# Kernel optimization log

Hardware: AMD Instinct MI355X
Metric: run time of the kernel (lower is better)

## Reference

```python
import jax, jax.numpy as jnp
import numpy as np

N, E, DIN, DH, DOUT = 50000, 800000, 256, 128, 64


def setup_inputs() -> dict:
    key = jax.random.key(0)
    ks = jax.random.split(key, 12)
    return {
        "h": jax.random.normal(ks[0], (N, DIN), jnp.float32),
        "src": jax.random.randint(ks[1], (E,), 0, N, jnp.int32),
        "dst": jax.random.randint(ks[2], (E,), 0, N, jnp.int32),
        "W1": jax.random.normal(ks[3], (DIN, DH), jnp.float32) * (DIN ** -0.5),
        "al1": jax.random.normal(ks[4], (DH,), jnp.float32) * (DH ** -0.5),
        "ar1": jax.random.normal(ks[5], (DH,), jnp.float32) * (DH ** -0.5),
        "W2": jax.random.normal(ks[6], (DH, DH), jnp.float32) * (DH ** -0.5),
        "al2": jax.random.normal(ks[7], (DH,), jnp.float32) * (DH ** -0.5),
        "ar2": jax.random.normal(ks[8], (DH,), jnp.float32) * (DH ** -0.5),
        "W3": jax.random.normal(ks[9], (DH, DOUT), jnp.float32) * (DH ** -0.5),
        "al3": jax.random.normal(ks[10], (DOUT,), jnp.float32) * (DOUT ** -0.5),
        "ar3": jax.random.normal(ks[11], (DOUT,), jnp.float32) * (DOUT ** -0.5),
    }


def gat_layer(h, W, al, ar, src, dst):
    """DGL GATConv, 1 head, no bias: proj -> leaky_relu edge scores -> edge softmax over dst -> scatter-sum."""
    n = h.shape[0]
    f = h @ W                                   # [N, d]
    el = f @ al                                 # [N]
    er = f @ ar                                 # [N]
    e = jax.nn.leaky_relu(el[src] + er[dst], negative_slope=0.2)  # [E]
    m = jax.ops.segment_max(e, dst, num_segments=n)
    m = jnp.where(jnp.isfinite(m), m, 0.0)      # zero-in-degree nodes
    m = jax.lax.stop_gradient(m)
    ex = jnp.exp(e - m[dst])                    # [E]
    z = jax.ops.segment_sum(ex, dst, num_segments=n)
    a = ex / jnp.maximum(z, 1e-9)[dst]          # [E] softmax weights
    return jax.ops.segment_sum(a[:, None] * f[src], dst, num_segments=n)


def reference(h, src, dst, W1, al1, ar1, W2, al2, ar2, W3, al3, ar3):
    x = gat_layer(h, W1, al1, ar1, src, dst)
    x = jax.nn.relu(x)                          # dropout = identity (eval)
    x = gat_layer(x, W2, al2, ar2, src, dst)
    x = jax.nn.relu(x)
    x = gat_layer(x, W3, al3, ar3, src, dst)    # mean over 1 head = identity
    return jax.nn.log_softmax(x, axis=-1)
```

## Files before the change

### kernel.cpp

```cpp
#include <hip/hip_runtime.h>
#include <math.h>

#define DIN 256
#define DHID 128
#define DOUTC 64
#define EPB 2048

typedef __attribute__((ext_vector_type(8))) short short8;
typedef __attribute__((ext_vector_type(4))) float f32x4;

static __device__ __forceinline__ float wave_max(float v){
  #pragma unroll
  for (int o=1;o<64;o<<=1) v = fmaxf(v, __shfl_xor(v,o,64));
  return v;
}
static __device__ __forceinline__ float wave_sum(float v){
  #pragma unroll
  for (int o=1;o<64;o<<=1) v += __shfl_xor(v,o,64);
  return v;
}

static __device__ __forceinline__ unsigned short bf16_rne(float x){
  unsigned int u = __float_as_uint(x);
  return (unsigned short)((u + 0x7FFFu + ((u>>16)&1u)) >> 16);
}
static __device__ __forceinline__ float bf16_to_f32(unsigned short h){
  return __uint_as_float(((unsigned int)h)<<16);
}
static __device__ __forceinline__ float blo(unsigned int u){ return __uint_as_float(u<<16); }
static __device__ __forceinline__ float bhi(unsigned int u){ return __uint_as_float(u & 0xffff0000u); }

__global__ __launch_bounds__(256) void rs_hist(const int* __restrict__ dst,
    int* __restrict__ ghist, int E, int NB){
  __shared__ int h[256];
  const int t = threadIdx.x, blk = blockIdx.x;
  h[t] = 0; __syncthreads();
  const int base = blk*EPB;
  #pragma unroll
  for (int i=0;i<EPB/256;i++){
    int j = base + i*256 + t;
    if (j < E) atomicAdd(&h[dst[j]>>8], 1);
  }
  __syncthreads();
  ghist[t*NB + blk] = h[t];
}

__global__ __launch_bounds__(256) void rs_scan(int* __restrict__ ghist,
    int* __restrict__ btot, int NB){
  __shared__ int b[256];
  __shared__ int carry;
  const int hb = blockIdx.x, t = threadIdx.x;
  if (t==0) carry = 0;
  __syncthreads();
  for (int c0=0; c0<NB; c0+=256){
    int i = c0 + t;
    int v = (i<NB)? ghist[hb*NB+i] : 0;
    b[t] = v; __syncthreads();
    #pragma unroll
    for (int o=1;o<256;o<<=1){
      int x = (t>=o)? b[t-o] : 0;
      __syncthreads();
      b[t] += x;
      __syncthreads();
    }
    if (i<NB) ghist[hb*NB+i] = carry + b[t] - v;
    __syncthreads();
    if (t==255) carry += b[255];
    __syncthreads();
  }
  if (t==255) btot[hb] = carry;
}

__global__ __launch_bounds__(256) void rs_scan2(int* __restrict__ btot,
    int* __restrict__ offsets, int N, int E){
  __shared__ int b[256];
  const int t = threadIdx.x;
  int v = btot[t];
  b[t] = v; __syncthreads();
  #pragma unroll
  for (int o=1;o<256;o<<=1){
    int x = (t>=o)? b[t-o] : 0;
    __syncthreads();
    b[t] += x;
    __syncthreads();
  }
  btot[t] = b[t] - v;
  if (t==255){ btot[256] = E; offsets[N] = E; }
}

__global__ __launch_bounds__(256) void rs_scatter(const int* __restrict__ src,
    const int* __restrict__ dst, const int* __restrict__ ghist,
    const int* __restrict__ btot, uint2* __restrict__ ebuf, int E, int NB){
  __shared__ int cur[256];
  const int t = threadIdx.x, blk = blockIdx.x;
  cur[t] = ghist[t*NB + blk] + btot[t];
  __syncthreads();
  const int base = blk*EPB;
  #pragma unroll
  for (int i=0;i<EPB/256;i++){
    int j = base + i*256 + t;
    if (j < E){
      int d = dst[j];
      int pos = atomicAdd(&cur[d>>8], 1);
      ebuf[pos] = make_uint2((unsigned)src[j], (unsigned)d);
    }
  }
}

__global__ __launch_bounds__(256) void bucket_sort(const uint2* __restrict__ ebuf,
    const int* __restrict__ btot, int* __restrict__ offsets,
    int* __restrict__ srcs, int N){
  __shared__ int h[256];
  __shared__ int b[256];
  const int hb = blockIdx.x, t = threadIdx.x;
  const int b0 = btot[hb], b1 = btot[hb+1];
  h[t] = 0; __syncthreads();
  for (int j=b0+t; j<b1; j+=256) atomicAdd(&h[ebuf[j].y & 255u], 1);
  __syncthreads();
  int v = h[t];
  b[t] = v; __syncthreads();
  #pragma unroll
  for (int o=1;o<256;o<<=1){
    int x = (t>=o)? b[t-o] : 0;
    __syncthreads();
    b[t] += x;
    __syncthreads();
  }
  const int excl = b[t] - v;
  const int node = hb*256 + t;
  if (node < N) offsets[node] = b0 + excl;
  h[t] = excl;
  __syncthreads();
  for (int j=b0+t; j<b1; j+=256){
    uint2 e = ebuf[j];
    int pos = b0 + atomicAdd(&h[e.y & 255u], 1);
    srcs[pos] = (int)e.x;
  }
}

template<int K, int NC>
__global__ void pack_kernel(const float* __restrict__ W, unsigned short* __restrict__ Wp){
  constexpr int CT = NC/16, KT = K/32;
  int idx = blockIdx.x*256 + threadIdx.x;
  if (idx >= KT*CT*64) return;
  int l = idx & 63, t = idx >> 6;
  int ct = t % CT, kt = t / CT;
  int col = ct*16 + (l & 15);
  int k0 = kt*32 + (l >> 4)*8;
  unsigned short* dstp = Wp + (size_t)idx*8;
  #pragma unroll
  for (int j=0;j<8;j++)
    dstp[j] = bf16_rne(W[(size_t)(k0+j)*NC + col]);
}

template<int K, int NC>
__global__ __launch_bounds__(256) void gemm_v3(const float* __restrict__ A,
    const unsigned short* __restrict__ Wp,
    const float* __restrict__ al, const float* __restrict__ ar,
    unsigned short* __restrict__ Fb, float* __restrict__ el, float* __restrict__ er, int nrows)
{
  constexpr int CT = NC/16, KT = K/32;
  constexpr int CHUNK_KT = (32/CT) < KT ? (32/CT) : KT;
  constexpr int NCHUNK = KT / CHUNK_KT;
  constexpr int CHUNK_SHORTS = CHUNK_KT*CT*64*8;
  __shared__ unsigned short bsm[CHUNK_SHORTS];

  const int tid = threadIdx.x;
  const int lane = tid & 63;
  const int wid  = tid >> 6;
  const int row0 = blockIdx.x*64 + wid*16;
  const int c = lane & 15, g = lane >> 4;
  const int arow = row0 + c;
  const bool aok = arow < nrows;

  f32x4 acc[CT];
  #pragma unroll
  for (int i=0;i<CT;i++) acc[i] = (f32x4)0.f;

  for (int ch=0; ch<NCHUNK; ++ch){
    if (ch) __syncthreads();
    {
      const uint4* gsrc = (const uint4*)Wp + (size_t)ch*(CHUNK_SHORTS/8);
      uint4* ldst = (uint4*)bsm;
      #pragma unroll
      for (int i=0; i<CHUNK_SHORTS/8/256; ++i)
        ldst[i*256 + tid] = gsrc[i*256 + tid];
    }
    __syncthreads();

    #pragma unroll
    for (int ktl=0; ktl<CHUNK_KT; ++ktl){
      const int k0 = (ch*CHUNK_KT + ktl)*32 + g*8;
      float xs[8];
      if (aok){
        float4 v0 = *(const float4*)&A[(size_t)arow*K + k0];
        float4 v1 = *(const float4*)&A[(size_t)arow*K + k0 + 4];
        xs[0]=v0.x; xs[1]=v0.y; xs[2]=v0.z; xs[3]=v0.w;
        xs[4]=v1.x; xs[5]=v1.y; xs[6]=v1.z; xs[7]=v1.w;
      } else {
        #pragma unroll
        for (int j=0;j<8;j++) xs[j]=0.f;
      }
      short8 ahi, alo;
      #pragma unroll
      for (int j=0;j<8;j++){
        unsigned short hh = bf16_rne(xs[j]);
        ahi[j] = (short)hh;
        alo[j] = (short)bf16_rne(xs[j] - bf16_to_f32(hh));
      }
      #pragma unroll
      for (int ct=0; ct<CT; ++ct){
        short8 b = *(const short8*)&bsm[(ktl*CT+ct)*512 + lane*8];
        acc[ct] = __builtin_amdgcn_mfma_f32_16x16x32_bf16(ahi, b, acc[ct], 0,0,0);
        acc[ct] = __builtin_amdgcn_mfma_f32_16x16x32_bf16(alo, b, acc[ct], 0,0,0);
      }
    }
  }

  float alv[CT], arv[CT];
  #pragma unroll
  for (int ct=0;ct<CT;ct++){ alv[ct]=al[ct*16+c]; arv[ct]=ar[ct*16+c]; }
  #pragma unroll
  for (int j=0;j<4;j++){
    const int row = row0 + g*4 + j;
    const bool ok = row < nrows;
    float sl=0.f, sr=0.f;
    #pragma unroll
    for (int ct=0;ct<CT;ct++){
      float f = acc[ct][j];
      sl = fmaf(f, alv[ct], sl);
      sr = fmaf(f, arv[ct], sr);
      if (ok) Fb[(size_t)row*NC + ct*16 + c] = bf16_rne(f);
    }
    #pragma unroll
    for (int o=1;o<16;o<<=1){ sl += __shfl_xor(sl,o,64); sr += __shfl_xor(sr,o,64); }
    if (ok && c==0){ el[row]=sl; er[row]=sr; }
  }
}

template<int D, bool RELU, bool LOGSM>
__global__ __launch_bounds__(256) void agg3_kernel(const unsigned short* __restrict__ Fb,
    const float* __restrict__ el, const float* __restrict__ er,
    const int* __restrict__ offsets, const int* __restrict__ srcs,
    float* __restrict__ out, int N)
{
  constexpr int CPL = D/16;
  __shared__ float2 ws[4][64];
  const int wv = threadIdx.x >> 6;
  const int lane = threadIdx.x & 63;
  const int c16 = lane & 15, g = lane >> 4;
  const int v = blockIdx.x*4 + wv;
  if (v >= N) return;
  const int o0 = offsets[v], o1 = offsets[v+1];
  const float erv = er[v];

  float m = -INFINITY, z = 0.f;
  float acc[CPL];
  #pragma unroll
  for (int i=0;i<CPL;i++) acc[i]=0.f;

  for (int s0 = o0; s0 < o1; s0 += 64){
    const int j = s0 + lane;
    int sidx = 0; float e = -INFINITY;
    if (j < o1){
      sidx = srcs[j];
      float tv = el[sidx] + erv;
      e = (tv > 0.f) ? tv : 0.2f*tv;
    }
    const float nm = fmaxf(m, wave_max(e));
    const float scale = __expf(m - nm);
    const float wgt = __expf(e - nm);
    z = z*scale + wave_sum(wgt);
    #pragma unroll
    for (int i=0;i<CPL;i++) acc[i] *= scale;
    m = nm;
    ws[wv][lane] = make_float2(wgt, __int_as_float(sidx));
    __builtin_amdgcn_wave_barrier();

    const int cnt = min(64, o1 - s0);
    int t = g;
    if (D == 128){
      for (; t+4 < cnt; t += 8){
        float2 p0 = ws[wv][t], p1 = ws[wv][t+4];
        uint4 u0 = *((const uint4*)(Fb + (size_t)__float_as_int(p0.y)*128) + c16);
        uint4 u1 = *((const uint4*)(Fb + (size_t)__float_as_int(p1.y)*128) + c16);
        acc[0]=fmaf(p0.x, blo(u0.x), acc[0]); acc[1]=fmaf(p0.x, bhi(u0.x), acc[1]);
        acc[2]=fmaf(p0.x, blo(u0.y), acc[2]); acc[3]=fmaf(p0.x, bhi(u0.y), acc[3]);
        acc[4]=fmaf(p0.x, blo(u0.z), acc[4]); acc[5]=fmaf(p0.x, bhi(u0.z), acc[5]);
        acc[6]=fmaf(p0.x, blo(u0.w), acc[6]); acc[7]=fmaf(p0.x, bhi(u0.w), acc[7]);
        acc[0]=fmaf(p1.x, blo(u1.x), acc[0]); acc[1]=fmaf(p1.x, bhi(u1.x), acc[1]);
        acc[2]=fmaf(p1.x, blo(u1.y), acc[2]); acc[3]=fmaf(p1.x, bhi(u1.y), acc[3]);
        acc[4]=fmaf(p1.x, blo(u1.z), acc[4]); acc[5]=fmaf(p1.x, bhi(u1.z), acc[5]);
        acc[6]=fmaf(p1.x, blo(u1.w), acc[6]); acc[7]=fmaf(p1.x, bhi(u1.w), acc[7]);
      }
      if (t < cnt){
        float2 p0 = ws[wv][t];
        uint4 u0 = *((const uint4*)(Fb + (size_t)__float_as_int(p0.y)*128) + c16);
        acc[0]=fmaf(p0.x, blo(u0.x), acc[0]); acc[1]=fmaf(p0.x, bhi(u0.x), acc[1]);
        acc[2]=fmaf(p0.x, blo(u0.y), acc[2]); acc[3]=fmaf(p0.x, bhi(u0.y), acc[3]);
        acc[4]=fmaf(p0.x, blo(u0.z), acc[4]); acc[5]=fmaf(p0.x, bhi(u0.z), acc[5]);
        acc[6]=fmaf(p0.x, blo(u0.w), acc[6]); acc[7]=fmaf(p0.x, bhi(u0.w), acc[7]);
      }
    } else {
      for (; t+4 < cnt; t += 8){
        float2 p0 = ws[wv][t], p1 = ws[wv][t+4];
        uint2 u0 = *((const uint2*)(Fb + (size_t)__float_as_int(p0.y)*64) + c16);
        uint2 u1 = *((const uint2*)(Fb + (size_t)__float_as_int(p1.y)*64) + c16);
        acc[0]=fmaf(p0.x, blo(u0.x), acc[0]); acc[1]=fmaf(p0.x, bhi(u0.x), acc[1]);
        acc[2]=fmaf(p0.x, blo(u0.y), acc[2]); acc[3]=fmaf(p0.x, bhi(u0.y), acc[3]);
        acc[0]=fmaf(p1.x, blo(u1.x), acc[0]); acc[1]=fmaf(p1.x, bhi(u1.x), acc[1]);
        acc[2]=fmaf(p1.x, blo(u1.y), acc[2]); acc[3]=fmaf(p1.x, bhi(u1.y), acc[3]);
      }
      if (t < cnt){
        float2 p0 = ws[wv][t];
        uint2 u0 = *((const uint2*)(Fb + (size_t)__float_as_int(p0.y)*64) + c16);
        acc[0]=fmaf(p0.x, blo(u0.x), acc[0]); acc[1]=fmaf(p0.x, bhi(u0.x), acc[1]);
        acc[2]=fmaf(p0.x, blo(u0.y), acc[2]); acc[3]=fmaf(p0.x, bhi(u0.y), acc[3]);
      }
    }
    __builtin_amdgcn_wave_barrier();
  }

  #pragma unroll
  for (int i=0;i<CPL;i++){
    acc[i] += __shfl_xor(acc[i],16,64);
    acc[i] += __shfl_xor(acc[i],32,64);
  }
  const float zi = 1.f / fmaxf(z, 1e-9f);

  if (LOGSM){
    float y[CPL];
    #pragma unroll
    for (int i=0;i<CPL;i++) y[i] = acc[i]*zi;
    float M = y[0];
    #pragma unroll
    for (int i=1;i<CPL;i++) M = fmaxf(M, y[i]);
    #pragma unroll
    for (int o=1;o<16;o<<=1) M = fmaxf(M, __shfl_xor(M,o,64));
    float ssum = 0.f;
    #pragma unroll
    for (int i=0;i<CPL;i++) ssum += __expf(y[i]-M);
    #pragma unroll
    for (int o=1;o<16;o<<=1) ssum += __shfl_xor(ssum,o,64);
    const float lw = M + logf(ssum);
    if (g==0){
      float4 r = make_float4(y[0]-lw, y[1]-lw, y[2]-lw, y[3]-lw);
      *(float4*)&out[(size_t)v*64 + c16*4] = r;
    }
  } else {
    if (g==0){
      float r[CPL];
      #pragma unroll
      for (int i=0;i<CPL;i++){ r[i]=acc[i]*zi; if (RELU) r[i]=fmaxf(r[i],0.f); }
      *(float4*)&out[(size_t)v*128 + c16*8]     = make_float4(r[0],r[1],r[2],r[3]);
      *(float4*)&out[(size_t)v*128 + c16*8 + 4] = make_float4(r[4],r[5],r[6],r[7]);
    }
  }
}

extern "C" void kernel_launch(void* const* d_in, const int* in_sizes, int n_in,
                              void* d_out, int out_size, void* d_ws, size_t ws_size,
                              hipStream_t stream) {
  const float* h   = (const float*)d_in[0];
  const int*   src = (const int*)d_in[1];
  const int*   dst = (const int*)d_in[2];
  const float* W1  = (const float*)d_in[3];
  const float* al1 = (const float*)d_in[4];
  const float* ar1 = (const float*)d_in[5];
  const float* W2  = (const float*)d_in[6];
  const float* al2 = (const float*)d_in[7];
  const float* ar2 = (const float*)d_in[8];
  const float* W3  = (const float*)d_in[9];
  const float* al3 = (const float*)d_in[10];
  const float* ar3 = (const float*)d_in[11];

  const int N = in_sizes[0] / DIN;
  const int E = in_sizes[1];
  const int NB = (E + EPB - 1) / EPB;
  const int NHB = (N + 255) / 256;

  auto alignup = [](size_t x){ return (x + 255) & ~(size_t)255; };
  char* p = (char*)d_ws;
  int* offsets = (int*)p; p += alignup(((size_t)N+1)*4);
  int* srcs    = (int*)p; p += alignup((size_t)E*4);
  int* ghist   = (int*)p; p += alignup((size_t)256*NB*4);
  int* btot    = (int*)p; p += alignup(257*4);
  uint2* ebuf  = (uint2*)p; p += alignup((size_t)E*8);
  unsigned short* Fb = (unsigned short*)p; p += alignup((size_t)N*DHID*2);
  float* X     = (float*)p; p += alignup((size_t)N*DHID*4);
  float* el    = (float*)p; p += alignup((size_t)N*4);
  float* er    = (float*)p; p += alignup((size_t)N*4);
  unsigned short* Wp1 = (unsigned short*)p; p += alignup((size_t)(DIN/32)*(DHID/16)*64*8*2);
  unsigned short* Wp2 = (unsigned short*)p; p += alignup((size_t)(DHID/32)*(DHID/16)*64*8*2);
  unsigned short* Wp3 = (unsigned short*)p; p += alignup((size_t)(DHID/32)*(DOUTC/16)*64*8*2);

  const int nbW4 = (N+3)/4;
  const int nbG  = (N+63)/64;

  pack_kernel<DIN ,DHID ><<<(DIN/32)*(DHID/16)*64/256,  256,0,stream>>>(W1, Wp1);
  pack_kernel<DHID,DHID ><<<(DHID/32)*(DHID/16)*64/256, 256,0,stream>>>(W2, Wp2);
  pack_kernel<DHID,DOUTC><<<(DHID/32)*(DOUTC/16)*64/256,256,0,stream>>>(W3, Wp3);

  rs_hist   <<<NB, 256,0,stream>>>(dst, ghist, E, NB);
  rs_scan   <<<256,256,0,stream>>>(ghist, btot, NB);
  rs_scan2  <<<1,  256,0,stream>>>(btot, offsets, N, E);
  rs_scatter<<<NB, 256,0,stream>>>(src, dst, ghist, btot, ebuf, E, NB);
  bucket_sort<<<NHB,256,0,stream>>>(ebuf, btot, offsets, srcs, N);

  gemm_v3<DIN,DHID><<<nbG,256,0,stream>>>(h, Wp1, al1, ar1, Fb, el, er, N);
  agg3_kernel<128,true,false><<<nbW4,256,0,stream>>>(Fb, el, er, offsets, srcs, X, N);

  gemm_v3<DHID,DHID><<<nbG,256,0,stream>>>(X, Wp2, al2, ar2, Fb, el, er, N);
  agg3_kernel<128,true,false><<<nbW4,256,0,stream>>>(Fb, el, er, offsets, srcs, X, N);

  gemm_v3<DHID,DOUTC><<<nbG,256,0,stream>>>(X, Wp3, al3, ar3, Fb, el, er, N);
  agg3_kernel<64,false,true><<<nbW4,256,0,stream>>>(Fb, el, er, offsets, srcs, (float*)d_out, N);
}
```

Baseline: 180.3 us.

## Store hidden activations in bf16, drop split-bf16 MFMA for layers 2-3, fuse weight packing

The intermediate activations X are now written as bf16 by the aggregation kernel. The layer 2 and 3 GEMMs read bf16 directly and issue one MFMA per tile instead of a hi/lo split pair. This halves activation traffic and GEMM MFMA work for those layers, at the cost of lower activation precision. The three weight-pack launches are merged into one kernel, and the gather loop is unrolled to four edges per iteration for more memory-level parallelism.

```diff
diff --git a/kernel.cpp b/kernel.cpp
--- a/kernel.cpp
+++ b/kernel.cpp
@@ -139,10 +139,9 @@
 }
 
 template<int K, int NC>
-__global__ void pack_kernel(const float* __restrict__ W, unsigned short* __restrict__ Wp){
-  constexpr int CT = NC/16, KT = K/32;
-  int idx = blockIdx.x*256 + threadIdx.x;
-  if (idx >= KT*CT*64) return;
+static __device__ __forceinline__ void pack_one(const float* __restrict__ W,
+    unsigned short* __restrict__ Wp, int idx){
+  constexpr int CT = NC/16;
   int l = idx & 63, t = idx >> 6;
   int ct = t % CT, kt = t / CT;
   int col = ct*16 + (l & 15);
@@ -153,8 +152,21 @@
     dstp[j] = bf16_rne(W[(size_t)(k0+j)*NC + col]);
 }
 
-template<int K, int NC>
-__global__ __launch_bounds__(256) void gemm_v3(const float* __restrict__ A,
+__global__ __launch_bounds__(256) void pack_all(const float* __restrict__ W1,
+    const float* __restrict__ W2, const float* __restrict__ W3,
+    unsigned short* __restrict__ Wp1, unsigned short* __restrict__ Wp2,
+    unsigned short* __restrict__ Wp3){
+  constexpr int N1 = (DIN/32)*(DHID/16)*64;
+  constexpr int N2 = (DHID/32)*(DHID/16)*64;
+  constexpr int N3 = (DHID/32)*(DOUTC/16)*64;
+  int idx = blockIdx.x*256 + threadIdx.x;
+  if (idx < N1) pack_one<DIN,DHID>(W1, Wp1, idx);
+  else if (idx < N1+N2) pack_one<DHID,DHID>(W2, Wp2, idx-N1);
+  else if (idx < N1+N2+N3) pack_one<DHID,DOUTC>(W3, Wp3, idx-N1-N2);
+}
+
+template<int K, int NC, bool AF32>
+__global__ __launch_bounds__(256) void gemm_v3(const void* __restrict__ Av,
     const unsigned short* __restrict__ Wp,
     const float* __restrict__ al, const float* __restrict__ ar,
     unsigned short* __restrict__ Fb, float* __restrict__ el, float* __restrict__ er, int nrows)
@@ -165,6 +177,9 @@
   constexpr int CHUNK_SHORTS = CHUNK_KT*CT*64*8;
   __shared__ unsigned short bsm[CHUNK_SHORTS];
 
+  const float* Af = (const float*)Av;
+  const unsigned short* Abf = (const unsigned short*)Av;
+
   const int tid = threadIdx.x;
   const int lane = tid & 63;
   const int wid  = tid >> 6;
@@ -191,28 +206,35 @@
     #pragma unroll
     for (int ktl=0; ktl<CHUNK_KT; ++ktl){
       const int k0 = (ch*CHUNK_KT + ktl)*32 + g*8;
-      float xs[8];
-      if (aok){
-        float4 v0 = *(const float4*)&A[(size_t)arow*K + k0];
-        float4 v1 = *(const float4*)&A[(size_t)arow*K + k0 + 4];
-        xs[0]=v0.x; xs[1]=v0.y; xs[2]=v0.z; xs[3]=v0.w;
-        xs[4]=v1.x; xs[5]=v1.y; xs[6]=v1.z; xs[7]=v1.w;
+      short8 ahi, alo;
+      if constexpr (AF32){
+        float xs[8];
+        if (aok){
+          float4 v0 = *(const float4*)&Af[(size_t)arow*K + k0];
+          float4 v1 = *(const float4*)&Af[(size_t)arow*K + k0 + 4];
+          xs[0]=v0.x; xs[1]=v0.y; xs[2]=v0.z; xs[3]=v0.w;
+          xs[4]=v1.x; xs[5]=v1.y; xs[6]=v1.z; xs[7]=v1.w;
+        } else {
+          #pragma unroll
+          for (int j=0;j<8;j++) xs[j]=0.f;
+        }
+        #pragma unroll
+        for (int j=0;j<8;j++){
+          unsigned short hh = bf16_rne(xs[j]);
+          ahi[j] = (short)hh;
+          alo[j] = (short)bf16_rne(xs[j] - bf16_to_f32(hh));
+        }
       } else {
-        #pragma unroll
-        for (int j=0;j<8;j++) xs[j]=0.f;
-      }
-      short8 ahi, alo;
-      #pragma unroll
-      for (int j=0;j<8;j++){
-        unsigned short hh = bf16_rne(xs[j]);
-        ahi[j] = (short)hh;
-        alo[j] = (short)bf16_rne(xs[j] - bf16_to_f32(hh));
+        if (aok) ahi = *(const short8*)&Abf[(size_t)arow*K + k0];
+        else     ahi = (short8)0;
+        alo = ahi;
       }
       #pragma unroll
       for (int ct=0; ct<CT; ++ct){
         short8 b = *(const short8*)&bsm[(ktl*CT+ct)*512 + lane*8];
         acc[ct] = __builtin_amdgcn_mfma_f32_16x16x32_bf16(ahi, b, acc[ct], 0,0,0);
-        acc[ct] = __builtin_amdgcn_mfma_f32_16x16x32_bf16(alo, b, acc[ct], 0,0,0);
+        if constexpr (AF32)
+          acc[ct] = __builtin_amdgcn_mfma_f32_16x16x32_bf16(alo, b, acc[ct], 0,0,0);
       }
     }
   }
@@ -238,11 +260,11 @@
   }
 }
 
-template<int D, bool RELU, bool LOGSM>
-__global__ __launch_bounds__(256) void agg3_kernel(const unsigned short* __restrict__ Fb,
+template<int D, bool RELU, bool LOGSM, bool OUTBF>
+__global__ __launch_bounds__(256) void agg4_kernel(const unsigned short* __restrict__ Fb,
     const float* __restrict__ el, const float* __restrict__ er,
     const int* __restrict__ offsets, const int* __restrict__ srcs,
-    float* __restrict__ out, int N)
+    void* __restrict__ outv, int N)
 {
   constexpr int CPL = D/16;
   __shared__ float2 ws[4][64];
@@ -279,11 +301,14 @@
 
     const int cnt = min(64, o1 - s0);
     int t = g;
-    if (D == 128){
-      for (; t+4 < cnt; t += 8){
-        float2 p0 = ws[wv][t], p1 = ws[wv][t+4];
+    if constexpr (D == 128){
+      for (; t+12 < cnt; t += 16){
+        float2 p0 = ws[wv][t],   p1 = ws[wv][t+4];
+        float2 p2 = ws[wv][t+8], p3 = ws[wv][t+12];
         uint4 u0 = *((const uint4*)(Fb + (size_t)__float_as_int(p0.y)*128) + c16);
         uint4 u1 = *((const uint4*)(Fb + (size_t)__float_as_int(p1.y)*128) + c16);
+        uint4 u2 = *((const uint4*)(Fb + (size_t)__float_as_int(p2.y)*128) + c16);
+        uint4 u3 = *((const uint4*)(Fb + (size_t)__float_as_int(p3.y)*128) + c16);
         acc[0]=fmaf(p0.x, blo(u0.x), acc[0]); acc[1]=fmaf(p0.x, bhi(u0.x), acc[1]);
         acc[2]=fmaf(p0.x, blo(u0.y), acc[2]); acc[3]=fmaf(p0.x, bhi(u0.y), acc[3]);
         acc[4]=fmaf(p0.x, blo(u0.z), acc[4]); acc[5]=fmaf(p0.x, bhi(u0.z), acc[5]);
@@ -292,8 +317,16 @@
         acc[2]=fmaf(p1.x, blo(u1.y), acc[2]); acc[3]=fmaf(p1.x, bhi(u1.y), acc[3]);
         acc[4]=fmaf(p1.x, blo(u1.z), acc[4]); acc[5]=fmaf(p1.x, bhi(u1.z), acc[5]);
         acc[6]=fmaf(p1.x, blo(u1.w), acc[6]); acc[7]=fmaf(p1.x, bhi(u1.w), acc[7]);
-      }
-      if (t < cnt){
+        acc[0]=fmaf(p2.x, blo(u2.x), acc[0]); acc[1]=fmaf(p2.x, bhi(u2.x), acc[1]);
+        acc[2]=fmaf(p2.x, blo(u2.y), acc[2]); acc[3]=fmaf(p2.x, bhi(u2.y), acc[3]);
+        acc[4]=fmaf(p2.x, blo(u2.z), acc[4]); acc[5]=fmaf(p2.x, bhi(u2.z), acc[5]);
+        acc[6]=fmaf(p2.x, blo(u2.w), acc[6]); acc[7]=fmaf(p2.x, bhi(u2.w), acc[7]);
+        acc[0]=fmaf(p3.x, blo(u3.x), acc[0]); acc[1]=fmaf(p3.x, bhi(u3.x), acc[1]);
+        acc[2]=fmaf(p3.x, blo(u3.y), acc[2]); acc[3]=fmaf(p3.x, bhi(u3.y), acc[3]);
+        acc[4]=fmaf(p3.x, blo(u3.z), acc[4]); acc[5]=fmaf(p3.x, bhi(u3.z), acc[5]);
+        acc[6]=fmaf(p3.x, blo(u3.w), acc[6]); acc[7]=fmaf(p3.x, bhi(u3.w), acc[7]);
+      }
+      for (; t < cnt; t += 4){
         float2 p0 = ws[wv][t];
         uint4 u0 = *((const uint4*)(Fb + (size_t)__float_as_int(p0.y)*128) + c16);
         acc[0]=fmaf(p0.x, blo(u0.x), acc[0]); acc[1]=fmaf(p0.x, bhi(u0.x), acc[1]);
@@ -302,16 +335,23 @@
         acc[6]=fmaf(p0.x, blo(u0.w), acc[6]); acc[7]=fmaf(p0.x, bhi(u0.w), acc[7]);
       }
     } else {
-      for (; t+4 < cnt; t += 8){
-        float2 p0 = ws[wv][t], p1 = ws[wv][t+4];
+      for (; t+12 < cnt; t += 16){
+        float2 p0 = ws[wv][t],   p1 = ws[wv][t+4];
+        float2 p2 = ws[wv][t+8], p3 = ws[wv][t+12];
         uint2 u0 = *((const uint2*)(Fb + (size_t)__float_as_int(p0.y)*64) + c16);
         uint2 u1 = *((const uint2*)(Fb + (size_t)__float_as_int(p1.y)*64) + c16);
+        uint2 u2 = *((const uint2*)(Fb + (size_t)__float_as_int(p2.y)*64) + c16);
+        uint2 u3 = *((const uint2*)(Fb + (size_t)__float_as_int(p3.y)*64) + c16);
         acc[0]=fmaf(p0.x, blo(u0.x), acc[0]); acc[1]=fmaf(p0.x, bhi(u0.x), acc[1]);
         acc[2]=fmaf(p0.x, blo(u0.y), acc[2]); acc[3]=fmaf(p0.x, bhi(u0.y), acc[3]);
         acc[0]=fmaf(p1.x, blo(u1.x), acc[0]); acc[1]=fmaf(p1.x, bhi(u1.x), acc[1]);
         acc[2]=fmaf(p1.x, blo(u1.y), acc[2]); acc[3]=fmaf(p1.x, bhi(u1.y), acc[3]);
-      }
-      if (t < cnt){
+        acc[0]=fmaf(p2.x, blo(u2.x), acc[0]); acc[1]=fmaf(p2.x, bhi(u2.x), acc[1]);
+        acc[2]=fmaf(p2.x, blo(u2.y), acc[2]); acc[3]=fmaf(p2.x, bhi(u2.y), acc[3]);
+        acc[0]=fmaf(p3.x, blo(u3.x), acc[0]); acc[1]=fmaf(p3.x, bhi(u3.x), acc[1]);
+        acc[2]=fmaf(p3.x, blo(u3.y), acc[2]); acc[3]=fmaf(p3.x, bhi(u3.y), acc[3]);
+      }
+      for (; t < cnt; t += 4){
         float2 p0 = ws[wv][t];
         uint2 u0 = *((const uint2*)(Fb + (size_t)__float_as_int(p0.y)*64) + c16);
         acc[0]=fmaf(p0.x, blo(u0.x), acc[0]); acc[1]=fmaf(p0.x, bhi(u0.x), acc[1]);
@@ -328,7 +368,8 @@
   }
   const float zi = 1.f / fmaxf(z, 1e-9f);
 
-  if (LOGSM){
+  if constexpr (LOGSM){
+    float* out = (float*)outv;
     float y[CPL];
     #pragma unroll
     for (int i=0;i<CPL;i++) y[i] = acc[i]*zi;
@@ -347,13 +388,17 @@
       float4 r = make_float4(y[0]-lw, y[1]-lw, y[2]-lw, y[3]-lw);
       *(float4*)&out[(size_t)v*64 + c16*4] = r;
     }
-  } else {
+  } else if constexpr (OUTBF){
+    unsigned short* outb = (unsigned short*)outv;
     if (g==0){
-      float r[CPL];
+      short8 o8;
       #pragma unroll
-      for (int i=0;i<CPL;i++){ r[i]=acc[i]*zi; if (RELU) r[i]=fmaxf(r[i],0.f); }
-      *(float4*)&out[(size_t)v*128 + c16*8]     = make_float4(r[0],r[1],r[2],r[3]);
-      *(float4*)&out[(size_t)v*128 + c16*8 + 4] = make_float4(r[4],r[5],r[6],r[7]);
+      for (int i=0;i<CPL;i++){
+        float r = acc[i]*zi;
+        if (RELU) r = fmaxf(r,0.f);
+        o8[i] = (short)bf16_rne(r);
+      }
+      *(short8*)&outb[(size_t)v*128 + c16*8] = o8;
     }
   }
 }
@@ -387,7 +432,7 @@
   int* btot    = (int*)p; p += alignup(257*4);
   uint2* ebuf  = (uint2*)p; p += alignup((size_t)E*8);
   unsigned short* Fb = (unsigned short*)p; p += alignup((size_t)N*DHID*2);
-  float* X     = (float*)p; p += alignup((size_t)N*DHID*4);
+  unsigned short* X  = (unsigned short*)p; p += alignup((size_t)N*DHID*2);
   float* el    = (float*)p; p += alignup((size_t)N*4);
   float* er    = (float*)p; p += alignup((size_t)N*4);
   unsigned short* Wp1 = (unsigned short*)p; p += alignup((size_t)(DIN/32)*(DHID/16)*64*8*2);
@@ -397,9 +442,7 @@
   const int nbW4 = (N+3)/4;
   const int nbG  = (N+63)/64;
 
-  pack_kernel<DIN ,DHID ><<<(DIN/32)*(DHID/16)*64/256,  256,0,stream>>>(W1, Wp1);
-  pack_kernel<DHID,DHID ><<<(DHID/32)*(DHID/16)*64/256, 256,0,stream>>>(W2, Wp2);
-  pack_kernel<DHID,DOUTC><<<(DHID/32)*(DOUTC/16)*64/256,256,0,stream>>>(W3, Wp3);
+  pack_all<<<28,256,0,stream>>>(W1, W2, W3, Wp1, Wp2, Wp3);
 
   rs_hist   <<<NB, 256,0,stream>>>(dst, ghist, E, NB);
   rs_scan   <<<256,256,0,stream>>>(ghist, btot, NB);
@@ -407,12 +450,12 @@
   rs_scatter<<<NB, 256,0,stream>>>(src, dst, ghist, btot, ebuf, E, NB);
   bucket_sort<<<NHB,256,0,stream>>>(ebuf, btot, offsets, srcs, N);
 
-  gemm_v3<DIN,DHID><<<nbG,256,0,stream>>>(h, Wp1, al1, ar1, Fb, el, er, N);
-  agg3_kernel<128,true,false><<<nbW4,256,0,stream>>>(Fb, el, er, offsets, srcs, X, N);
-
-  gemm_v3<DHID,DHID><<<nbG,256,0,stream>>>(X, Wp2, al2, ar2, Fb, el, er, N);
-  agg3_kernel<128,true,false><<<nbW4,256,0,stream>>>(Fb, el, er, offsets, srcs, X, N);
-
-  gemm_v3<DHID,DOUTC><<<nbG,256,0,stream>>>(X, Wp3, al3, ar3, Fb, el, er, N);
-  agg3_kernel<64,false,true><<<nbW4,256,0,stream>>>(Fb, el, er, offsets, srcs, (float*)d_out, N);
-}
+  gemm_v3<DIN,DHID,true><<<nbG,256,0,stream>>>(h, Wp1, al1, ar1, Fb, el, er, N);
+  agg4_kernel<128,true,false,true><<<nbW4,256,0,stream>>>(Fb, el, er, offsets, srcs, X, N);
+
+  gemm_v3<DHID,DHID,false><<<nbG,256,0,stream>>>(X, Wp2, al2, ar2, Fb, el, er, N);
+  agg4_kernel<128,true,false,true><<<nbW4,256,0,stream>>>(Fb, el, er, offsets, srcs, X, N);
+
+  gemm_v3<DHID,DOUTC,false><<<nbG,256,0,stream>>>(X, Wp3, al3, ar3, Fb, el, er, N);
+  agg4_kernel<64,false,true,false><<<nbW4,256,0,stream>>>(Fb, el, er, offsets, srcs, d_out, N);
+}
```

Result: slower. 185.7 us (+3.0%).
